# Performance work log

Hardware: AMD Instinct MI355X
Metric: run time of the kernel (lower is better)

## Reference

```python
import jax, jax.numpy as jnp
import numpy as np
import math

B, S, E, R = 128, 16, 512, 500  # batch, seq_len, emb_size, relation_num


def setup_inputs() -> dict:
    key = jax.random.key(0)
    ks = jax.random.split(key, 12)
    s = 1.0 / math.sqrt(E)
    emb = jax.random.normal(ks[0], (R + 1, E), jnp.float32) * s
    emb = emb.at[R].set(0.0)  # padding_idx row is zero in torch
    w_ih = jax.random.normal(ks[1], (4 * E, E), jnp.float32) * s
    w_hh = jax.random.normal(ks[2], (4 * E, E), jnp.float32) * s
    b_ih = jax.random.normal(ks[3], (4 * E,), jnp.float32) * s
    b_hh = jax.random.normal(ks[4], (4 * E,), jnp.float32) * s
    fc_w = jax.random.normal(ks[5], (1, E), jnp.float32) * s
    fc_b = jax.random.normal(ks[6], (1,), jnp.float32) * s
    fcq_w = jax.random.normal(ks[7], (E, E), jnp.float32) * s
    fcq_b = jax.random.normal(ks[8], (E,), jnp.float32) * s
    fck_w = jax.random.normal(ks[9], (E, E), jnp.float32) * s
    fck_b = jax.random.normal(ks[10], (E,), jnp.float32) * s
    tokens = jax.random.randint(ks[11], (B, S), 0, R)  # avoid padding idx R
    return dict(tokens=tokens, emb=emb, w_ih=w_ih, w_hh=w_hh, b_ih=b_ih,
                b_hh=b_hh, fc_w=fc_w, fc_b=fc_b, fcq_w=fcq_w, fcq_b=fcq_b,
                fck_w=fck_w, fck_b=fck_b)


def _lstm_pair(x, w_ih, w_hh, b):
    # x: [..., 2, E]; 2-step LSTM from zero state, return final hidden [..., E]
    def cell(xt, h, c):
        g = xt @ w_ih.T + h @ w_hh.T + b
        i, f, gg, o = jnp.split(g, 4, axis=-1)  # torch gate order i,f,g,o
        c = jax.nn.sigmoid(f) * c + jax.nn.sigmoid(i) * jnp.tanh(gg)
        return jax.nn.sigmoid(o) * jnp.tanh(c), c
    z = jnp.zeros_like(x[..., 0, :])
    h1, c1 = cell(x[..., 0, :], z, z)
    h2, _ = cell(x[..., 1, :], h1, c1)
    return h2


def _attention(x, rel_emb, fcq_w, fcq_b, fck_w, fck_b):
    # x: [B,q,E]; keys = [relation embeddings ; x] -> scores [B,q,R+q]
    b = x.shape[0]
    rel = jnp.broadcast_to(rel_emb[None], (b,) + rel_emb.shape)
    kin = jnp.concatenate([rel, x], axis=1)
    k = kin @ fck_w.T + fck_b
    q = x @ fcq_w.T + fcq_b
    return jnp.einsum('bqe,bke->bqk', q, k) / math.sqrt(E)


def _entropy(scores):
    lp = jax.nn.log_softmax(scores, axis=-1)
    return -jnp.sum(jnp.exp(lp) * lp, axis=-1)


def reference(tokens, emb, w_ih, w_hh, b_ih, b_hh, fc_w, fc_b,
              fcq_w, fcq_b, fck_w, fck_b):
    b_lstm = b_ih + b_hh
    rel_emb = emb[:R]  # relation embeddings used as attention keys/values
    cur = emb[tokens]  # [B,S,E]
    bidx = jnp.arange(B)
    losses = []
    for L in range(S, 1, -1):  # lengths processed: S, S-1, ..., 2
        if L > 2:
            # all adjacent pairs, batched 2-step LSTM: [B, L-1, E]
            pairs = jnp.stack([cur[:, :-1], cur[:, 1:]], axis=2)
            h = _lstm_pair(pairs, w_ih, w_hh, b_lstm)
            sc = jax.nn.sigmoid(h @ fc_w.T + fc_b)[..., 0]  # [B, L-1]
            sel = jnp.argmax(sc, axis=-1)  # [B]
            selected = jnp.take_along_axis(h, sel[:, None, None], axis=1)  # [B,1,E]
            scores = _attention(selected, rel_emb, fcq_w, fcq_b, fck_w, fck_b)
            losses.append(_entropy(scores))  # [B,1]
            # weightedAverage: mask is all-False for seq_len==1, plain softmax
            prob = jax.nn.softmax(scores, axis=-1)  # [B,1,R+1]
            all_emb = jnp.concatenate(
                [jnp.broadcast_to(rel_emb[None], (B, R, E)), selected], axis=1)
            merged = jnp.einsum('bqk,bke->bqe', prob, all_emb)[:, 0]  # [B,E]
            # output = inputs.detach().clone(); write merged at sel; drop row sel+1
            base = jax.lax.stop_gradient(cur)
            base = base.at[bidx, sel].set(merged)
            j = jnp.arange(L - 1)[None, :]
            src = j + (j > sel[:, None]).astype(j.dtype)
            cur = jnp.take_along_axis(base, src[:, :, None], axis=1)  # [B,L-1,E]
        else:  # L == 2: plain LSTM over the two tokens
            h = _lstm_pair(cur, w_ih, w_hh, b_lstm)  # [B,E]
            cur = h[:, None, :]
            losses.append(jnp.zeros((B, 1), cur.dtype))
    scores_f = _attention(cur, rel_emb, fcq_w, fcq_b, fck_w, fck_b)  # [B,1,R+1]
    losses.append(_entropy(scores_f))
    loss_tensor = jnp.concatenate(losses, axis=-1)  # [B,S]
    return scores_f[:, 0], loss_tensor
```

## Files before the change

kernel.cpp:

```cpp
#include <hip/hip_runtime.h>
#include <hip/hip_bf16.h>

#define BB 128
#define SS 16
#define EE 512
#define RR 500
#define G4 2048
#define OUT0 64128
#define NSC 501
#define NPAIR 2047
#define NSU 1012

__device__ __forceinline__ float sigm(float x) { return 1.f / (1.f + expf(-x)); }

__device__ float g_blstm[G4];
__device__ float g_fcw[EE + 4];
__device__ float g_qbias[1024];
__device__ float g_Krel[RR * EE];
__device__ float g_cur[BB * SS * EE];
__device__ float g_G[BB * SS * G4];
__device__ float g_h1[BB * SS * EE];
__device__ float g_c1[BB * SS * EE];
__device__ float g_h2[BB * SS * EE];
__device__ float g_g2[BB * SS * G4];
__device__ float g_sc[BB * SS];
__device__ float g_ent[BB * SS];
__device__ int   g_sel[BB];
__device__ int   g_ord[BB * SS];
__device__ float g_fckwT[EE * EE];
__device__ float g_W2[RR * EE];
__device__ float g_Mx[EE * EE];
__device__ float g_c2[RR + 4];
__device__ float g_v1[EE];
__device__ float g_c0[1];
__device__ float g_su[BB * NSU];

__global__ void k_prep(const float* __restrict__ bih, const float* __restrict__ bhh,
                       const float* __restrict__ fcwv, const float* __restrict__ fcbv,
                       const float* __restrict__ fcqb, const float* __restrict__ fckb) {
    int i = blockIdx.x * blockDim.x + threadIdx.x;
    if (i < G4) g_blstm[i] = bih[i] + bhh[i];
    if (i < EE) {
        g_fcw[i] = fcwv[i];
        g_qbias[i] = fcqb[i];
        g_qbias[EE + i] = fckb[i];
    }
    if (i == 0) g_fcw[EE] = fcbv[0];
    if (i < BB * SS) g_ord[i] = i;
}

__global__ void k_gather(const int* __restrict__ tok, const float* __restrict__ emb) {
    int i = blockIdx.x * blockDim.x + threadIdx.x;
    if (i >= BB * SS * EE) return;
    int e = i & (EE - 1);
    int r = i >> 9;
    int t = tok[r];
    g_cur[i] = emb[(size_t)t * EE + e];
}

__global__ void k_tr(const float* __restrict__ fckw) {
    int i = blockIdx.x * blockDim.x + threadIdx.x;
    if (i >= EE * EE) return;
    int ep = i >> 9;
    int f = i & (EE - 1);
    g_fckwT[(size_t)f * EE + ep] = fckw[(size_t)ep * EE + f];
}

__global__ __launch_bounds__(512) void k_vprep(const float* __restrict__ fcqw, const float* __restrict__ fckw) {
    __shared__ float sh[512];
    int t = threadIdx.x;
    int blk = blockIdx.x;
    if (blk == 0) {
        float acc = 0.f;
        for (int ep = 0; ep < EE; ep++)
            acc += g_qbias[ep] * fckw[(size_t)ep * EE + t] + g_qbias[EE + ep] * fcqw[(size_t)ep * EE + t];
        g_v1[t] = acc;
    } else if (blk == 1) {
        sh[t] = g_qbias[t] * g_qbias[EE + t];
        __syncthreads();
        for (int s = 256; s > 0; s >>= 1) { if (t < s) sh[t] += sh[t + s]; __syncthreads(); }
        if (t == 0) g_c0[0] = sh[0];
    } else {
        int k = blk - 2;
        sh[t] = g_Krel[(size_t)k * EE + t] * g_qbias[t];
        __syncthreads();
        for (int s = 256; s > 0; s >>= 1) { if (t < s) sh[t] += sh[t + s]; __syncthreads(); }
        if (t == 0) g_c2[k] = sh[0];
    }
}

#define TM 32
#define TN 64
#define TK 32
__device__ __forceinline__ void gemm_dev(
    const float* __restrict__ A, int lda,
    const float* __restrict__ W, int ldw, int wtrans,
    const float* __restrict__ bias, const float* __restrict__ Dadd, int ldd,
    float* __restrict__ C, int ldc, int M, int N, int K)
{
    __shared__ __align__(16) float As[TK][TM + 2];
    __shared__ __align__(16) float Ws[TK][TN + 4];
    int tid = threadIdx.x;
    int mt = blockIdx.y * TM;
    int nt = blockIdx.x * TN;
    int tr = tid >> 4;
    int tc = tid & 15;
    float acc[2][4] = {{0.f,0.f,0.f,0.f},{0.f,0.f,0.f,0.f}};

    int ea = tid * 4;
    int ra = ea >> 5;
    int ka = ea & 31;
    int gmA = mt + ra;
    bool rokA = gmA < M;
    int ew = tid * 8;
    int rw = ew >> 5;
    int kw = ew & 31;
    int gnW = nt + rw;
    bool rokW = gnW < N;

    for (int kt = 0; kt < K; kt += TK) {
        #pragma unroll
        for (int i = 0; i < 4; i++) {
            int gk = kt + ka + i;
            float v = 0.f;
            if (rokA && gk < K) v = A[(size_t)gmA * lda + gk];
            As[ka + i][ra] = v;
        }
        #pragma unroll
        for (int i = 0; i < 8; i++) {
            int gk = kt + kw + i;
            float v = 0.f;
            if (rokW && gk < K)
                v = wtrans ? W[(size_t)gk * ldw + gnW] : W[(size_t)gnW * ldw + gk];
            Ws[kw + i][rw] = v;
        }
        __syncthreads();
        #pragma unroll
        for (int kk = 0; kk < TK; kk++) {
            const float2 a = *(const float2*)&As[kk][2 * tr];
            const float4 w = *(const float4*)&Ws[kk][4 * tc];
            acc[0][0] += a.x * w.x; acc[0][1] += a.x * w.y; acc[0][2] += a.x * w.z; acc[0][3] += a.x * w.w;
            acc[1][0] += a.y * w.x; acc[1][1] += a.y * w.y; acc[1][2] += a.y * w.z; acc[1][3] += a.y * w.w;
        }
        __syncthreads();
    }
    #pragma unroll
    for (int i = 0; i < 2; i++) {
        int gm = mt + 2 * tr + i;
        if (gm >= M) continue;
        #pragma unroll
        for (int j = 0; j < 4; j++) {
            int gn = nt + 4 * tc + j;
            if (gn >= N) continue;
            float v = (i == 0) ? ((j == 0) ? acc[0][0] : (j == 1) ? acc[0][1] : (j == 2) ? acc[0][2] : acc[0][3])
                               : ((j == 0) ? acc[1][0] : (j == 1) ? acc[1][1] : (j == 2) ? acc[1][2] : acc[1][3]);
            if (bias) v += bias[gn];
            if (Dadd) v += Dadd[(size_t)gm * ldd + gn];
            C[(size_t)gm * ldc + gn] = v;
        }
    }
}

__global__ __launch_bounds__(256) void kg_Krel(const float* __restrict__ emb, const float* __restrict__ fckw) {
    gemm_dev(emb, EE, fckw, EE, 0, g_qbias + EE, nullptr, 0, g_Krel, EE, RR, EE, EE);
}
__global__ __launch_bounds__(256) void kg_W2(const float* __restrict__ fcqw) {
    gemm_dev(g_Krel, EE, fcqw, EE, 1, nullptr, nullptr, 0, g_W2, EE, RR, EE, EE);
}
__global__ __launch_bounds__(256) void kg_Mx(const float* __restrict__ fcqw) {
    gemm_dev(g_fckwT, EE, fcqw, EE, 1, nullptr, nullptr, 0, g_Mx, EE, EE, EE, EE);
}
__global__ __launch_bounds__(256) void kg_G(const float* __restrict__ wih) {
    gemm_dev(g_cur, EE, wih, EE, 0, g_blstm, nullptr, 0, g_G, G4, BB * SS, G4, EE);
}
__global__ __launch_bounds__(256) void kg_g2(const float* __restrict__ whh) {
    gemm_dev(g_h1, EE, whh, EE, 0, nullptr, g_G + G4, G4, g_g2, G4, NPAIR, G4, EE);
}

__global__ __launch_bounds__(256) void kg_su(int P) {
    __shared__ __align__(16) float As[TK][TM + 2];
    __shared__ __align__(16) float Ws[TK][TN + 4];
    __shared__ int s_phys[TM];
    int tid = threadIdx.x;
    int mt = blockIdx.y * TM;
    int nt = blockIdx.x * TN;
    int tr = tid >> 4;
    int tc = tid & 15;
    float acc[2][4] = {{0.f,0.f,0.f,0.f},{0.f,0.f,0.f,0.f}};

    if (tid < TM) {
        int b = mt + tid;
        float best = -1e30f; int bi = 0;
        for (int p = 0; p < P; p++) {
            float v = g_sc[b * SS + p];
            if (v > best) { best = v; bi = p; }
        }
        s_phys[tid] = g_ord[b * SS + bi];
        if (blockIdx.x == 0) g_sel[b] = bi;
    }
    __syncthreads();

    int ea = tid * 4;
    int ra = ea >> 5;
    int ka = ea & 31;
    int physA = s_phys[ra];
    int ew = tid * 8;
    int rw = ew >> 5;
    int kw = ew & 31;
    int gnW = nt + rw;
    bool rokW = gnW < NSU;
    const float* Wrow = nullptr;
    if (rokW) Wrow = (gnW < RR) ? (g_W2 + (size_t)gnW * EE) : (g_Mx + (size_t)(gnW - RR) * EE);

    for (int kt = 0; kt < EE; kt += TK) {
        #pragma unroll
        for (int i = 0; i < 4; i++)
            As[ka + i][ra] = g_h2[(size_t)physA * EE + kt + ka + i];
        #pragma unroll
        for (int i = 0; i < 8; i++)
            Ws[kw + i][rw] = rokW ? Wrow[kt + kw + i] : 0.f;
        __syncthreads();
        #pragma unroll
        for (int kk = 0; kk < TK; kk++) {
            const float2 a = *(const float2*)&As[kk][2 * tr];
            const float4 w = *(const float4*)&Ws[kk][4 * tc];
            acc[0][0] += a.x * w.x; acc[0][1] += a.x * w.y; acc[0][2] += a.x * w.z; acc[0][3] += a.x * w.w;
            acc[1][0] += a.y * w.x; acc[1][1] += a.y * w.y; acc[1][2] += a.y * w.z; acc[1][3] += a.y * w.w;
        }
        __syncthreads();
    }
    #pragma unroll
    for (int i = 0; i < 2; i++) {
        int gm = mt + 2 * tr + i;
        #pragma unroll
        for (int j = 0; j < 4; j++) {
            int gn = nt + 4 * tc + j;
            if (gn >= NSU) continue;
            float v = (i == 0) ? ((j == 0) ? acc[0][0] : (j == 1) ? acc[0][1] : (j == 2) ? acc[0][2] : acc[0][3])
                               : ((j == 0) ? acc[1][0] : (j == 1) ? acc[1][1] : (j == 2) ? acc[1][2] : acc[1][3]);
            g_su[(size_t)gm * NSU + gn] = v + (gn < RR ? g_c2[gn] : 0.f);
        }
    }
}

__global__ __launch_bounds__(256) void kg_Gi(const float* __restrict__ wih) {
    __shared__ __align__(16) float As[TK][TM + 2];
    __shared__ __align__(16) float Ws[TK][TN + 4];
    __shared__ int s_phys[TM];
    int tid = threadIdx.x;
    int mt = blockIdx.y * TM;
    int nt = blockIdx.x * TN;
    int tr = tid >> 4;
    int tc = tid & 15;
    float acc[2][4] = {{0.f,0.f,0.f,0.f},{0.f,0.f,0.f,0.f}};

    if (tid < TM) {
        int b = mt + tid;
        s_phys[tid] = g_ord[b * SS + g_sel[b]];
    }
    __syncthreads();

    int ea = tid * 4;
    int ra = ea >> 5;
    int ka = ea & 31;
    int physA = s_phys[ra];
    int ew = tid * 8;
    int rw = ew >> 5;
    int kw = ew & 31;
    int gnW = nt + rw;

    for (int kt = 0; kt < EE; kt += TK) {
        #pragma unroll
        for (int i = 0; i < 4; i++)
            As[ka + i][ra] = g_cur[(size_t)physA * EE + kt + ka + i];
        #pragma unroll
        for (int i = 0; i < 8; i++)
            Ws[kw + i][rw] = wih[(size_t)gnW * EE + kt + kw + i];
        __syncthreads();
        #pragma unroll
        for (int kk = 0; kk < TK; kk++) {
            const float2 a = *(const float2*)&As[kk][2 * tr];
            const float4 w = *(const float4*)&Ws[kk][4 * tc];
            acc[0][0] += a.x * w.x; acc[0][1] += a.x * w.y; acc[0][2] += a.x * w.z; acc[0][3] += a.x * w.w;
            acc[1][0] += a.y * w.x; acc[1][1] += a.y * w.y; acc[1][2] += a.y * w.z; acc[1][3] += a.y * w.w;
        }
        __syncthreads();
    }
    #pragma unroll
    for (int i = 0; i < 2; i++) {
        int phys = s_phys[2 * tr + i];
        #pragma unroll
        for (int j = 0; j < 4; j++) {
            int gn = nt + 4 * tc + j;
            float v = (i == 0) ? ((j == 0) ? acc[0][0] : (j == 1) ? acc[0][1] : (j == 2) ? acc[0][2] : acc[0][3])
                               : ((j == 0) ? acc[1][0] : (j == 1) ? acc[1][1] : (j == 2) ? acc[1][2] : acc[1][3]);
            g_G[(size_t)phys * G4 + gn] = v + g_blstm[gn];
        }
    }
}

__global__ void k_h1i() {
    int idx = blockIdx.x * blockDim.x + threadIdx.x;
    if (idx >= BB * EE) return;
    int b = idx >> 9;
    int e = idx & (EE - 1);
    int phys = g_ord[b * SS + g_sel[b]];
    const float* g = g_G + (size_t)phys * G4;
    float c = sigm(g[e]) * tanhf(g[1024 + e]);
    g_c1[(size_t)phys * EE + e] = c;
    g_h1[(size_t)phys * EE + e] = sigm(g[1536 + e]) * tanhf(c);
}

__global__ __launch_bounds__(256) void kg_g2i(const float* __restrict__ whh) {
    __shared__ __align__(16) float As[TK][TM + 2];
    __shared__ __align__(16) float Ws[TK][TN + 4];
    __shared__ int s_physA[TM];
    __shared__ int s_physD[TM];
    int tid = threadIdx.x;
    int mt = blockIdx.y * TM;
    int nt = blockIdx.x * TN;
    int tr = tid >> 4;
    int tc = tid & 15;
    float acc[2][4] = {{0.f,0.f,0.f,0.f},{0.f,0.f,0.f,0.f}};

    if (tid < TM) {
        int gm = mt + tid;
        int b = gm >> 1;
        int p = min(max(g_sel[b] - 1 + (gm & 1), 0), 14);
        s_physA[tid] = g_ord[b * SS + p];
        s_physD[tid] = g_ord[b * SS + p + 1];
    }
    __syncthreads();

    int ea = tid * 4;
    int ra = ea >> 5;
    int ka = ea & 31;
    int physA = s_physA[ra];
    int ew = tid * 8;
    int rw = ew >> 5;
    int kw = ew & 31;
    int gnW = nt + rw;

    for (int kt = 0; kt < EE; kt += TK) {
        #pragma unroll
        for (int i = 0; i < 4; i++)
            As[ka + i][ra] = g_h1[(size_t)physA * EE + kt + ka + i];
        #pragma unroll
        for (int i = 0; i < 8; i++)
            Ws[kw + i][rw] = whh[(size_t)gnW * EE + kt + kw + i];
        __syncthreads();
        #pragma unroll
        for (int kk = 0; kk < TK; kk++) {
            const float2 a = *(const float2*)&As[kk][2 * tr];
            const float4 w = *(const float4*)&Ws[kk][4 * tc];
            acc[0][0] += a.x * w.x; acc[0][1] += a.x * w.y; acc[0][2] += a.x * w.z; acc[0][3] += a.x * w.w;
            acc[1][0] += a.y * w.x; acc[1][1] += a.y * w.y; acc[1][2] += a.y * w.z; acc[1][3] += a.y * w.w;
        }
        __syncthreads();
    }
    #pragma unroll
    for (int i = 0; i < 2; i++) {
        int gm = mt + 2 * tr + i;
        size_t drow = (size_t)s_physD[2 * tr + i] * G4;
        #pragma unroll
        for (int j = 0; j < 4; j++) {
            int gn = nt + 4 * tc + j;
            float v = (i == 0) ? ((j == 0) ? acc[0][0] : (j == 1) ? acc[0][1] : (j == 2) ? acc[0][2] : acc[0][3])
                               : ((j == 0) ? acc[1][0] : (j == 1) ? acc[1][1] : (j == 2) ? acc[1][2] : acc[1][3]);
            g_g2[(size_t)gm * G4 + gn] = v + g_G[drow + gn];
        }
    }
}

__global__ void k_h1() {
    int idx = blockIdx.x * blockDim.x + threadIdx.x;
    if (idx >= BB * SS * EE) return;
    int m = idx >> 9;
    int e = idx & (EE - 1);
    const float* g = g_G + (size_t)m * G4;
    float c = sigm(g[e]) * tanhf(g[1024 + e]);
    g_c1[idx] = c;
    g_h1[idx] = sigm(g[1536 + e]) * tanhf(c);
}

__global__ __launch_bounds__(256) void k_h2() {
    int m = blockIdx.x;
    const float* g = g_g2 + (size_t)m * G4;
    __shared__ float red[256];
    float part = 0.f;
    for (int e = threadIdx.x; e < EE; e += 256) {
        float c = sigm(g[512 + e]) * g_c1[(size_t)m * EE + e] + sigm(g[e]) * tanhf(g[1024 + e]);
        float h = sigm(g[1536 + e]) * tanhf(c);
        g_h2[(size_t)m * EE + e] = h;
        part += h * g_fcw[e];
    }
    red[threadIdx.x] = part;
    __syncthreads();
    for (int s = 128; s > 0; s >>= 1) {
        if (threadIdx.x < s) red[threadIdx.x] += red[threadIdx.x + s];
        __syncthreads();
    }
    if (threadIdx.x == 0) g_sc[m] = sigm(red[0] + g_fcw[EE]);
}

__global__ __launch_bounds__(256) void k_h2i(int L) {
    int m = blockIdx.x;
    int b = m >> 1;
    int t = m & 1;
    int s = g_sel[b];
    int p = s - 1 + t;
    bool valid = t == 0 ? (s >= 1) : (s <= L - 3);
    if (!valid) return;
    int physL = g_ord[b * SS + p];
    const float* g = g_g2 + (size_t)m * G4;
    __shared__ float red[256];
    float part = 0.f;
    for (int e = threadIdx.x; e < EE; e += 256) {
        float c = sigm(g[512 + e]) * g_c1[(size_t)physL * EE + e] + sigm(g[e]) * tanhf(g[1024 + e]);
        float h = sigm(g[1536 + e]) * tanhf(c);
        g_h2[(size_t)physL * EE + e] = h;
        part += h * g_fcw[e];
    }
    red[threadIdx.x] = part;
    __syncthreads();
    for (int ss = 128; ss > 0; ss >>= 1) {
        if (threadIdx.x < ss) red[threadIdx.x] += red[threadIdx.x + ss];
        __syncthreads();
    }
    if (threadIdx.x == 0) g_sc[b * SS + p] = sigm(red[0] + g_fcw[EE]);
}

__global__ __launch_bounds__(512) void k_smu(int col, int finalFlag, int L,
                                             const float* __restrict__ emb, float* __restrict__ out) {
    int b = blockIdx.x;
    int t = threadIdx.x;
    __shared__ float sh[512];
    __shared__ float srow[NSC];
    __shared__ float s_p500;
    const float* su = g_su + (size_t)b * NSU;
    int s = g_sel[b];
    int phys = g_ord[b * SS + s];
    const float* h2row = g_h2 + (size_t)phys * EE;
    const float isq = 0.044194173824159216f;

    float hv = h2row[t];
    sh[t] = hv * (su[RR + t] + g_v1[t]);
    __syncthreads();
    for (int ss = 256; ss > 0; ss >>= 1) { if (t < ss) sh[t] += sh[t + ss]; __syncthreads(); }
    if (t == 0) srow[RR] = (sh[0] + g_c0[0]) * isq;
    __syncthreads();
    if (t < RR) srow[t] = su[t] * isq;
    __syncthreads();
    float mx = (t < NSC) ? srow[t] : -1e30f;
    sh[t] = mx; __syncthreads();
    for (int ss = 256; ss > 0; ss >>= 1) { if (t < ss) sh[t] = fmaxf(sh[t], sh[t + ss]); __syncthreads(); }
    mx = sh[0]; __syncthreads();
    float zp = (t < NSC) ? expf(srow[t] - mx) : 0.f;
    sh[t] = zp; __syncthreads();
    for (int ss = 256; ss > 0; ss >>= 1) { if (t < ss) sh[t] += sh[t + ss]; __syncthreads(); }
    float lse = mx + logf(sh[0]);
    __syncthreads();
    float p = (t < NSC) ? expf(srow[t] - lse) : 0.f;
    float ep = (t < NSC) ? p * (lse - srow[t]) : 0.f;
    if (finalFlag && t < NSC) out[(size_t)b * NSC + t] = srow[t];
    sh[t] = ep; __syncthreads();
    for (int ss = 256; ss > 0; ss >>= 1) { if (t < ss) sh[t] += sh[t + ss]; __syncthreads(); }
    if (finalFlag) {
        if (t < 16) {
            float v = (t == 15) ? sh[0] : ((t == 14) ? 0.f : g_ent[b * SS + t]);
            out[OUT0 + b * 16 + t] = v;
        }
        return;
    }
    if (t == 0) g_ent[b * SS + col] = sh[0];

    __syncthreads();
    if (t < NSC) srow[t] = p;
    if (t == RR) s_p500 = p;
    __syncthreads();
    float macc = 0.f;
    #pragma unroll 4
    for (int k = 0; k < RR; k++) macc += srow[k] * emb[(size_t)k * EE + t];
    g_cur[(size_t)phys * EE + t] = macc + s_p500 * hv;
    if (t == 0) {
        for (int j = s + 1; j <= L - 2; j++) g_ord[b * SS + j] = g_ord[b * SS + j + 1];
        for (int pp = s + 1; pp <= L - 3; pp++) g_sc[b * SS + pp] = g_sc[b * SS + pp + 1];
    }
}

extern "C" void kernel_launch(void* const* d_in, const int* in_sizes, int n_in,
                              void* d_out, int out_size, void* d_ws, size_t ws_size,
                              hipStream_t stream) {
    const int*   tokens = (const int*)d_in[0];
    const float* emb    = (const float*)d_in[1];
    const float* wih    = (const float*)d_in[2];
    const float* whh    = (const float*)d_in[3];
    const float* bih    = (const float*)d_in[4];
    const float* bhh    = (const float*)d_in[5];
    const float* fcwv   = (const float*)d_in[6];
    const float* fcbv   = (const float*)d_in[7];
    const float* fcqw   = (const float*)d_in[8];
    const float* fcqb   = (const float*)d_in[9];
    const float* fckw   = (const float*)d_in[10];
    const float* fckb   = (const float*)d_in[11];
    float* out = (float*)d_out;

    auto grid32 = [](int M, int N) { return dim3((unsigned)((N + TN - 1) / TN), (unsigned)((M + TM - 1) / TM)); };

    k_prep<<<dim3(8), dim3(256), 0, stream>>>(bih, bhh, fcwv, fcbv, fcqb, fckb);
    kg_Krel<<<grid32(RR, EE), dim3(256), 0, stream>>>(emb, fckw);
    k_tr<<<dim3((EE * EE + 255) / 256), dim3(256), 0, stream>>>(fckw);
    kg_W2<<<grid32(RR, EE), dim3(256), 0, stream>>>(fcqw);
    kg_Mx<<<grid32(EE, EE), dim3(256), 0, stream>>>(fcqw);
    k_vprep<<<dim3(502), dim3(512), 0, stream>>>(fcqw, fckw);
    k_gather<<<dim3((BB * SS * EE + 255) / 256), dim3(256), 0, stream>>>(tokens, emb);

    kg_G<<<grid32(BB * SS, G4), dim3(256), 0, stream>>>(wih);
    k_h1<<<dim3((BB * SS * EE + 255) / 256), dim3(256), 0, stream>>>();
    kg_g2<<<grid32(NPAIR, G4), dim3(256), 0, stream>>>(whh);
    k_h2<<<dim3(NPAIR), dim3(256), 0, stream>>>();

    for (int L = SS; L >= 3; L--) {
        kg_su<<<grid32(BB, NSU), dim3(256), 0, stream>>>(L - 1);
        k_smu<<<dim3(BB), dim3(512), 0, stream>>>(SS - L, 0, L, emb, out);
        kg_Gi<<<grid32(BB, G4), dim3(256), 0, stream>>>(wih);
        k_h1i<<<dim3((BB * EE + 255) / 256), dim3(256), 0, stream>>>();
        kg_g2i<<<grid32(2 * BB, G4), dim3(256), 0, stream>>>(whh);
        k_h2i<<<dim3(2 * BB), dim3(256), 0, stream>>>(L);
    }

    kg_su<<<grid32(BB, NSU), dim3(256), 0, stream>>>(1);
    k_smu<<<dim3(BB), dim3(512), 0, stream>>>(15, 1, 2, emb, out);

    (void)in_sizes; (void)n_in; (void)out_size; (void)d_ws; (void)ws_size;
}
```

Before: 2.051 ms.

## Use 128x128 register-blocked GEMM tiles for the large LSTM gate GEMMs

```diff
diff --git a/kernel.cpp b/kernel.cpp
--- a/kernel.cpp
+++ b/kernel.cpp
@@ -161,6 +161,102 @@
     }
 }
 
+#define UM 128
+#define UN 128
+#define UK 32
+__device__ __forceinline__ void gemm_dev128(
+    const float* __restrict__ A, int lda,
+    const float* __restrict__ W, int ldw,
+    const float* __restrict__ bias, const float* __restrict__ Dadd, int ldd,
+    float* __restrict__ C, int ldc, int M, int N, int K)
+{
+    __shared__ __align__(16) float As[UK][UM + 4];
+    __shared__ __align__(16) float Ws[UK][UN + 4];
+    int tid = threadIdx.x;
+    int mt = blockIdx.y * UM;
+    int nt = blockIdx.x * UN;
+    int tr = tid >> 4;
+    int tc = tid & 15;
+    float acc[8][8] = {};
+
+    int ra = tid & 127;
+    int ka = (tid >> 7) << 4;
+    int gmA = mt + ra;
+    bool rokA = gmA < M;
+    int gnW = nt + ra;
+    bool rokW = gnW < N;
+    const float* Arow = A + (size_t)(rokA ? gmA : 0) * lda;
+    const float* Wrow = W + (size_t)(rokW ? gnW : 0) * ldw;
+
+    for (int kt = 0; kt < K; kt += UK) {
+        if (rokA) {
+            const float4 a0 = *(const float4*)&Arow[kt + ka];
+            const float4 a1 = *(const float4*)&Arow[kt + ka + 4];
+            const float4 a2 = *(const float4*)&Arow[kt + ka + 8];
+            const float4 a3 = *(const float4*)&Arow[kt + ka + 12];
+            As[ka +  0][ra] = a0.x; As[ka +  1][ra] = a0.y; As[ka +  2][ra] = a0.z; As[ka +  3][ra] = a0.w;
+            As[ka +  4][ra] = a1.x; As[ka +  5][ra] = a1.y; As[ka +  6][ra] = a1.z; As[ka +  7][ra] = a1.w;
+            As[ka +  8][ra] = a2.x; As[ka +  9][ra] = a2.y; As[ka + 10][ra] = a2.z; As[ka + 11][ra] = a2.w;
+            As[ka + 12][ra] = a3.x; As[ka + 13][ra] = a3.y; As[ka + 14][ra] = a3.z; As[ka + 15][ra] = a3.w;
+        } else {
+            #pragma unroll
+            for (int i = 0; i < 16; i++) As[ka + i][ra] = 0.f;
+        }
+        if (rokW) {
+            const float4 w0 = *(const float4*)&Wrow[kt + ka];
+            const float4 w1 = *(const float4*)&Wrow[kt + ka + 4];
+            const float4 w2 = *(const float4*)&Wrow[kt + ka + 8];
+            const float4 w3 = *(const float4*)&Wrow[kt + ka + 12];
+            Ws[ka +  0][ra] = w0.x; Ws[ka +  1][ra] = w0.y; Ws[ka +  2][ra] = w0.z; Ws[ka +  3][ra] = w0.w;
+            Ws[ka +  4][ra] = w1.x; Ws[ka +  5][ra] = w1.y; Ws[ka +  6][ra] = w1.z; Ws[ka +  7][ra] = w1.w;
+            Ws[ka +  8][ra] = w2.x; Ws[ka +  9][ra] = w2.y; Ws[ka + 10][ra] = w2.z; Ws[ka + 11][ra] = w2.w;
+            Ws[ka + 12][ra] = w3.x; Ws[ka + 13][ra] = w3.y; Ws[ka + 14][ra] = w3.z; Ws[ka + 15][ra] = w3.w;
+        } else {
+            #pragma unroll
+            for (int i = 0; i < 16; i++) Ws[ka + i][ra] = 0.f;
+        }
+        __syncthreads();
+        #pragma unroll
+        for (int kk = 0; kk < UK; kk++) {
+            const float4 aA = *(const float4*)&As[kk][8 * tr];
+            const float4 aB = *(const float4*)&As[kk][8 * tr + 4];
+            const float4 wA = *(const float4*)&Ws[kk][8 * tc];
+            const float4 wB = *(const float4*)&Ws[kk][8 * tc + 4];
+            const float am[8] = {aA.x, aA.y, aA.z, aA.w, aB.x, aB.y, aB.z, aB.w};
+            const float wn[8] = {wA.x, wA.y, wA.z, wA.w, wB.x, wB.y, wB.z, wB.w};
+            #pragma unroll
+            for (int i = 0; i < 8; i++)
+                #pragma unroll
+                for (int j = 0; j < 8; j++)
+                    acc[i][j] += am[i] * wn[j];
+        }
+        __syncthreads();
+    }
+
+    float4 b0 = {0.f, 0.f, 0.f, 0.f}, b1 = {0.f, 0.f, 0.f, 0.f};
+    int gn0 = nt + 8 * tc;
+    if (bias) {
+        b0 = *(const float4*)&bias[gn0];
+        b1 = *(const float4*)&bias[gn0 + 4];
+    }
+    #pragma unroll
+    for (int i = 0; i < 8; i++) {
+        int gm = mt + 8 * tr + i;
+        if (gm >= M) continue;
+        float4 v0, v1;
+        v0.x = acc[i][0] + b0.x; v0.y = acc[i][1] + b0.y; v0.z = acc[i][2] + b0.z; v0.w = acc[i][3] + b0.w;
+        v1.x = acc[i][4] + b1.x; v1.y = acc[i][5] + b1.y; v1.z = acc[i][6] + b1.z; v1.w = acc[i][7] + b1.w;
+        if (Dadd) {
+            const float4 d0 = *(const float4*)&Dadd[(size_t)gm * ldd + gn0];
+            const float4 d1 = *(const float4*)&Dadd[(size_t)gm * ldd + gn0 + 4];
+            v0.x += d0.x; v0.y += d0.y; v0.z += d0.z; v0.w += d0.w;
+            v1.x += d1.x; v1.y += d1.y; v1.z += d1.z; v1.w += d1.w;
+        }
+        *(float4*)&C[(size_t)gm * ldc + gn0] = v0;
+        *(float4*)&C[(size_t)gm * ldc + gn0 + 4] = v1;
+    }
+}
+
 __global__ __launch_bounds__(256) void kg_Krel(const float* __restrict__ emb, const float* __restrict__ fckw) {
     gemm_dev(emb, EE, fckw, EE, 0, g_qbias + EE, nullptr, 0, g_Krel, EE, RR, EE, EE);
 }
@@ -171,10 +267,10 @@
     gemm_dev(g_fckwT, EE, fcqw, EE, 1, nullptr, nullptr, 0, g_Mx, EE, EE, EE, EE);
 }
 __global__ __launch_bounds__(256) void kg_G(const float* __restrict__ wih) {
-    gemm_dev(g_cur, EE, wih, EE, 0, g_blstm, nullptr, 0, g_G, G4, BB * SS, G4, EE);
+    gemm_dev128(g_cur, EE, wih, EE, g_blstm, nullptr, 0, g_G, G4, BB * SS, G4, EE);
 }
 __global__ __launch_bounds__(256) void kg_g2(const float* __restrict__ whh) {
-    gemm_dev(g_h1, EE, whh, EE, 0, nullptr, g_G + G4, G4, g_g2, G4, NPAIR, G4, EE);
+    gemm_dev128(g_h1, EE, whh, EE, nullptr, g_G + G4, G4, g_g2, G4, NPAIR, G4, EE);
 }
 
 __global__ __launch_bounds__(256) void kg_su(int P) {
@@ -506,6 +602,7 @@
     float* out = (float*)d_out;
 
     auto grid32 = [](int M, int N) { return dim3((unsigned)((N + TN - 1) / TN), (unsigned)((M + TM - 1) / TM)); };
+    auto grid128 = [](int M, int N) { return dim3((unsigned)((N + UN - 1) / UN), (unsigned)((M + UM - 1) / UM)); };
 
     k_prep<<<dim3(8), dim3(256), 0, stream>>>(bih, bhh, fcwv, fcbv, fcqb, fckb);
     kg_Krel<<<grid32(RR, EE), dim3(256), 0, stream>>>(emb, fckw);
@@ -515,9 +612,9 @@
     k_vprep<<<dim3(502), dim3(512), 0, stream>>>(fcqw, fckw);
     k_gather<<<dim3((BB * SS * EE + 255) / 256), dim3(256), 0, stream>>>(tokens, emb);
 
-    kg_G<<<grid32(BB * SS, G4), dim3(256), 0, stream>>>(wih);
+    kg_G<<<grid128(BB * SS, G4), dim3(256), 0, stream>>>(wih);
     k_h1<<<dim3((BB * SS * EE + 255) / 256), dim3(256), 0, stream>>>();
-    kg_g2<<<grid32(NPAIR, G4), dim3(256), 0, stream>>>(whh);
+    kg_g2<<<grid128(NPAIR, G4), dim3(256), 0, stream>>>(whh);
     k_h2<<<dim3(NPAIR), dim3(256), 0, stream>>>();
 
     for (int L = SS; L >= 3; L--) {
```

Result: no change. 2.050 ms (-0.0%).

## Interleave LSTM gate weights to fuse cell updates into GEMM epilogues

Applied to the files above, without the earlier changes.

```diff
diff --git a/kernel.cpp b/kernel.cpp
--- a/kernel.cpp
+++ b/kernel.cpp
@@ -14,6 +14,9 @@
 __device__ __forceinline__ float sigm(float x) { return 1.f / (1.f + expf(-x)); }
 
 __device__ float g_blstm[G4];
+__device__ float g_blstmr[G4];
+__device__ float g_wihr[G4 * EE];
+__device__ float g_whhr[G4 * EE];
 __device__ float g_fcw[EE + 4];
 __device__ float g_qbias[1024];
 __device__ float g_Krel[RR * EE];
@@ -22,7 +25,6 @@
 __device__ float g_h1[BB * SS * EE];
 __device__ float g_c1[BB * SS * EE];
 __device__ float g_h2[BB * SS * EE];
-__device__ float g_g2[BB * SS * G4];
 __device__ float g_sc[BB * SS];
 __device__ float g_ent[BB * SS];
 __device__ int   g_sel[BB];
@@ -47,6 +49,19 @@
     }
     if (i == 0) g_fcw[EE] = fcbv[0];
     if (i < BB * SS) g_ord[i] = i;
+}
+
+__global__ void k_reord(const float* __restrict__ wih, const float* __restrict__ whh) {
+    int i = blockIdx.x * blockDim.x + threadIdx.x;
+    if (i >= G4 * EE) return;
+    int n = i >> 9;
+    int k = i & (EE - 1);
+    int e = n & (EE - 1);
+    int gate = n >> 9;
+    int np = 4 * e + gate;
+    g_wihr[(size_t)np * EE + k] = wih[i];
+    g_whhr[(size_t)np * EE + k] = whh[i];
+    if (k == 0) g_blstmr[np] = g_blstm[n];
 }
 
 __global__ void k_gather(const int* __restrict__ tok, const float* __restrict__ emb) {
@@ -161,6 +176,116 @@
     }
 }
 
+#define UM 128
+#define UN 128
+#define UK 32
+template<int MODE>
+__global__ __launch_bounds__(256) void kg_bigF() {
+    __shared__ __align__(16) float As[UK][UM + 4];
+    __shared__ __align__(16) float Ws[UK][UN + 4];
+    const float* __restrict__ A = (MODE == 0) ? g_cur : g_h1;
+    const float* __restrict__ W = (MODE == 0) ? g_wihr : g_whhr;
+    const int M = (MODE == 0) ? (BB * SS) : NPAIR;
+    int tid = threadIdx.x;
+    int mt = blockIdx.y * UM;
+    int nt = blockIdx.x * UN;
+    int tr = tid >> 4;
+    int tc = tid & 15;
+    float acc[8][8] = {};
+
+    int ra = tid & 127;
+    int ka = (tid >> 7) << 4;
+    int gmA = mt + ra;
+    bool rokA = gmA < M;
+    const float* Arow = A + (size_t)(rokA ? gmA : 0) * EE;
+    const float* Wrow = W + (size_t)(nt + ra) * EE;
+
+    float4 pa[4] = {{0,0,0,0},{0,0,0,0},{0,0,0,0},{0,0,0,0}};
+    float4 pw[4];
+    #pragma unroll
+    for (int j = 0; j < 4; j++) {
+        if (rokA) pa[j] = *(const float4*)&Arow[ka + 4 * j];
+        pw[j] = *(const float4*)&Wrow[ka + 4 * j];
+    }
+
+    for (int kt = 0; kt < EE; kt += UK) {
+        __syncthreads();
+        #pragma unroll
+        for (int j = 0; j < 4; j++) {
+            As[ka + 4 * j + 0][ra] = pa[j].x;
+            As[ka + 4 * j + 1][ra] = pa[j].y;
+            As[ka + 4 * j + 2][ra] = pa[j].z;
+            As[ka + 4 * j + 3][ra] = pa[j].w;
+            Ws[ka + 4 * j + 0][ra] = pw[j].x;
+            Ws[ka + 4 * j + 1][ra] = pw[j].y;
+            Ws[ka + 4 * j + 2][ra] = pw[j].z;
+            Ws[ka + 4 * j + 3][ra] = pw[j].w;
+        }
+        __syncthreads();
+        if (kt + UK < EE) {
+            int k2 = kt + UK + ka;
+            #pragma unroll
+            for (int j = 0; j < 4; j++) {
+                if (rokA) pa[j] = *(const float4*)&Arow[k2 + 4 * j];
+                pw[j] = *(const float4*)&Wrow[k2 + 4 * j];
+            }
+        }
+        #pragma unroll
+        for (int kk = 0; kk < UK; kk++) {
+            const float4 aA = *(const float4*)&As[kk][4 * tr];
+            const float4 aB = *(const float4*)&As[kk][64 + 4 * tr];
+            const float4 wA = *(const float4*)&Ws[kk][4 * tc];
+            const float4 wB = *(const float4*)&Ws[kk][64 + 4 * tc];
+            const float am[8] = {aA.x, aA.y, aA.z, aA.w, aB.x, aB.y, aB.z, aB.w};
+            const float wn[8] = {wA.x, wA.y, wA.z, wA.w, wB.x, wB.y, wB.z, wB.w};
+            #pragma unroll
+            for (int i = 0; i < 8; i++)
+                #pragma unroll
+                for (int j = 0; j < 8; j++)
+                    acc[i][j] += am[i] * wn[j];
+        }
+    }
+
+    int c0 = nt + 4 * tc;
+    int c1c = c0 + 64;
+    int e0 = (nt >> 2) + tc;
+    #pragma unroll
+    for (int ri = 0; ri < 8; ri++) {
+        int row = (ri < 4) ? (4 * tr + ri) : (60 + 4 * tr + ri);
+        int gm = mt + row;
+        if (gm >= M) continue;
+        float q0x = acc[ri][0], q0y = acc[ri][1], q0z = acc[ri][2], q0w = acc[ri][3];
+        float q1x = acc[ri][4], q1y = acc[ri][5], q1z = acc[ri][6], q1w = acc[ri][7];
+        if (MODE == 0) {
+            const float4 b0 = *(const float4*)&g_blstmr[c0];
+            const float4 b1 = *(const float4*)&g_blstmr[c1c];
+            q0x += b0.x; q0y += b0.y; q0z += b0.z; q0w += b0.w;
+            q1x += b1.x; q1y += b1.y; q1z += b1.z; q1w += b1.w;
+            float4 o0 = {q0x, q0y, q0z, q0w};
+            float4 o1 = {q1x, q1y, q1z, q1w};
+            *(float4*)&g_G[(size_t)gm * G4 + c0]  = o0;
+            *(float4*)&g_G[(size_t)gm * G4 + c1c] = o1;
+            float cA = sigm(q0x) * tanhf(q0z);
+            g_c1[(size_t)gm * EE + e0] = cA;
+            g_h1[(size_t)gm * EE + e0] = sigm(q0w) * tanhf(cA);
+            float cB = sigm(q1x) * tanhf(q1z);
+            g_c1[(size_t)gm * EE + e0 + 16] = cB;
+            g_h1[(size_t)gm * EE + e0 + 16] = sigm(q1w) * tanhf(cB);
+        } else {
+            const float4 d0 = *(const float4*)&g_G[(size_t)(gm + 1) * G4 + c0];
+            const float4 d1 = *(const float4*)&g_G[(size_t)(gm + 1) * G4 + c1c];
+            q0x += d0.x; q0y += d0.y; q0z += d0.z; q0w += d0.w;
+            q1x += d1.x; q1y += d1.y; q1z += d1.z; q1w += d1.w;
+            float c1a = g_c1[(size_t)gm * EE + e0];
+            float c1b = g_c1[(size_t)gm * EE + e0 + 16];
+            float cA = sigm(q0y) * c1a + sigm(q0x) * tanhf(q0z);
+            g_h2[(size_t)gm * EE + e0] = sigm(q0w) * tanhf(cA);
+            float cB = sigm(q1y) * c1b + sigm(q1x) * tanhf(q1z);
+            g_h2[(size_t)gm * EE + e0 + 16] = sigm(q1w) * tanhf(cB);
+        }
+    }
+}
+
 __global__ __launch_bounds__(256) void kg_Krel(const float* __restrict__ emb, const float* __restrict__ fckw) {
     gemm_dev(emb, EE, fckw, EE, 0, g_qbias + EE, nullptr, 0, g_Krel, EE, RR, EE, EE);
 }
@@ -170,11 +295,36 @@
 __global__ __launch_bounds__(256) void kg_Mx(const float* __restrict__ fcqw) {
     gemm_dev(g_fckwT, EE, fcqw, EE, 1, nullptr, nullptr, 0, g_Mx, EE, EE, EE, EE);
 }
-__global__ __launch_bounds__(256) void kg_G(const float* __restrict__ wih) {
-    gemm_dev(g_cur, EE, wih, EE, 0, g_blstm, nullptr, 0, g_G, G4, BB * SS, G4, EE);
-}
-__global__ __launch_bounds__(256) void kg_g2(const float* __restrict__ whh) {
-    gemm_dev(g_h1, EE, whh, EE, 0, nullptr, g_G + G4, G4, g_g2, G4, NPAIR, G4, EE);
+
+__global__ __launch_bounds__(256) void k_scI() {
+    int m = blockIdx.x;
+    int t = threadIdx.x;
+    __shared__ float red[256];
+    const float* h = g_h2 + (size_t)m * EE;
+    float part = h[t] * g_fcw[t] + h[t + 256] * g_fcw[t + 256];
+    red[t] = part;
+    __syncthreads();
+    for (int s = 128; s > 0; s >>= 1) { if (t < s) red[t] += red[t + s]; __syncthreads(); }
+    if (t == 0) g_sc[m] = red[0];
+}
+
+__global__ __launch_bounds__(256) void k_scP(int L) {
+    int m = blockIdx.x;
+    int b = m >> 1;
+    int tcand = m & 1;
+    int s = g_sel[b];
+    int p = s - 1 + tcand;
+    bool valid = tcand == 0 ? (s >= 1) : (s <= L - 3);
+    if (!valid) return;
+    int physL = g_ord[b * SS + p];
+    int t = threadIdx.x;
+    __shared__ float red[256];
+    const float* h = g_h2 + (size_t)physL * EE;
+    float part = h[t] * g_fcw[t] + h[t + 256] * g_fcw[t + 256];
+    red[t] = part;
+    __syncthreads();
+    for (int s2 = 128; s2 > 0; s2 >>= 1) { if (t < s2) red[t] += red[t + s2]; __syncthreads(); }
+    if (t == 0) g_sc[b * SS + p] = red[0];
 }
 
 __global__ __launch_bounds__(256) void kg_su(int P) {
@@ -243,7 +393,7 @@
     }
 }
 
-__global__ __launch_bounds__(256) void kg_Gi(const float* __restrict__ wih) {
+__global__ __launch_bounds__(256) void kg_GiF() {
     __shared__ __align__(16) float As[TK][TM + 2];
     __shared__ __align__(16) float Ws[TK][TN + 4];
     __shared__ int s_phys[TM];
@@ -275,7 +425,7 @@
             As[ka + i][ra] = g_cur[(size_t)physA * EE + kt + ka + i];
         #pragma unroll
         for (int i = 0; i < 8; i++)
-            Ws[kw + i][rw] = wih[(size_t)gnW * EE + kt + kw + i];
+            Ws[kw + i][rw] = g_wihr[(size_t)gnW * EE + kt + kw + i];
         __syncthreads();
         #pragma unroll
         for (int kk = 0; kk < TK; kk++) {
@@ -286,36 +436,30 @@
         }
         __syncthreads();
     }
+    int c0 = nt + 4 * tc;
+    int e0 = (nt >> 2) + tc;
+    const float4 b4 = *(const float4*)&g_blstmr[c0];
     #pragma unroll
     for (int i = 0; i < 2; i++) {
         int phys = s_phys[2 * tr + i];
-        #pragma unroll
-        for (int j = 0; j < 4; j++) {
-            int gn = nt + 4 * tc + j;
-            float v = (i == 0) ? ((j == 0) ? acc[0][0] : (j == 1) ? acc[0][1] : (j == 2) ? acc[0][2] : acc[0][3])
-                               : ((j == 0) ? acc[1][0] : (j == 1) ? acc[1][1] : (j == 2) ? acc[1][2] : acc[1][3]);
-            g_G[(size_t)phys * G4 + gn] = v + g_blstm[gn];
-        }
-    }
-}
-
-__global__ void k_h1i() {
-    int idx = blockIdx.x * blockDim.x + threadIdx.x;
-    if (idx >= BB * EE) return;
-    int b = idx >> 9;
-    int e = idx & (EE - 1);
-    int phys = g_ord[b * SS + g_sel[b]];
-    const float* g = g_G + (size_t)phys * G4;
-    float c = sigm(g[e]) * tanhf(g[1024 + e]);
-    g_c1[(size_t)phys * EE + e] = c;
-    g_h1[(size_t)phys * EE + e] = sigm(g[1536 + e]) * tanhf(c);
-}
-
-__global__ __launch_bounds__(256) void kg_g2i(const float* __restrict__ whh) {
+        float qx = acc[i][0] + b4.x;
+        float qy = acc[i][1] + b4.y;
+        float qz = acc[i][2] + b4.z;
+        float qw = acc[i][3] + b4.w;
+        float4 o = {qx, qy, qz, qw};
+        *(float4*)&g_G[(size_t)phys * G4 + c0] = o;
+        float cA = sigm(qx) * tanhf(qz);
+        g_c1[(size_t)phys * EE + e0] = cA;
+        g_h1[(size_t)phys * EE + e0] = sigm(qw) * tanhf(cA);
+    }
+}
+
+__global__ __launch_bounds__(256) void kg_g2iF(int L) {
     __shared__ __align__(16) float As[TK][TM + 2];
     __shared__ __align__(16) float Ws[TK][TN + 4];
     __shared__ int s_physA[TM];
     __shared__ int s_physD[TM];
+    __shared__ int s_val[TM];
     int tid = threadIdx.x;
     int mt = blockIdx.y * TM;
     int nt = blockIdx.x * TN;
@@ -326,9 +470,12 @@
     if (tid < TM) {
         int gm = mt + tid;
         int b = gm >> 1;
-        int p = min(max(g_sel[b] - 1 + (gm & 1), 0), 14);
+        int tcand = gm & 1;
+        int s = g_sel[b];
+        int p = min(max(s - 1 + tcand, 0), 14);
         s_physA[tid] = g_ord[b * SS + p];
         s_physD[tid] = g_ord[b * SS + p + 1];
+        s_val[tid] = tcand == 0 ? (s >= 1) : (s <= L - 3);
     }
     __syncthreads();
 
@@ -347,7 +494,7 @@
             As[ka + i][ra] = g_h1[(size_t)physA * EE + kt + ka + i];
         #pragma unroll
         for (int i = 0; i < 8; i++)
-            Ws[kw + i][rw] = whh[(size_t)gnW * EE + kt + kw + i];
+            Ws[kw + i][rw] = g_whhr[(size_t)gnW * EE + kt + kw + i];
         __syncthreads();
         #pragma unroll
         for (int kk = 0; kk < TK; kk++) {
@@ -358,76 +505,23 @@
         }
         __syncthreads();
     }
+    int c0 = nt + 4 * tc;
+    int e0 = (nt >> 2) + tc;
     #pragma unroll
     for (int i = 0; i < 2; i++) {
-        int gm = mt + 2 * tr + i;
-        size_t drow = (size_t)s_physD[2 * tr + i] * G4;
-        #pragma unroll
-        for (int j = 0; j < 4; j++) {
-            int gn = nt + 4 * tc + j;
-            float v = (i == 0) ? ((j == 0) ? acc[0][0] : (j == 1) ? acc[0][1] : (j == 2) ? acc[0][2] : acc[0][3])
-                               : ((j == 0) ? acc[1][0] : (j == 1) ? acc[1][1] : (j == 2) ? acc[1][2] : acc[1][3]);
-            g_g2[(size_t)gm * G4 + gn] = v + g_G[drow + gn];
-        }
-    }
-}
-
-__global__ void k_h1() {
-    int idx = blockIdx.x * blockDim.x + threadIdx.x;
-    if (idx >= BB * SS * EE) return;
-    int m = idx >> 9;
-    int e = idx & (EE - 1);
-    const float* g = g_G + (size_t)m * G4;
-    float c = sigm(g[e]) * tanhf(g[1024 + e]);
-    g_c1[idx] = c;
-    g_h1[idx] = sigm(g[1536 + e]) * tanhf(c);
-}
-
-__global__ __launch_bounds__(256) void k_h2() {
-    int m = blockIdx.x;
-    const float* g = g_g2 + (size_t)m * G4;
-    __shared__ float red[256];
-    float part = 0.f;
-    for (int e = threadIdx.x; e < EE; e += 256) {
-        float c = sigm(g[512 + e]) * g_c1[(size_t)m * EE + e] + sigm(g[e]) * tanhf(g[1024 + e]);
-        float h = sigm(g[1536 + e]) * tanhf(c);
-        g_h2[(size_t)m * EE + e] = h;
-        part += h * g_fcw[e];
-    }
-    red[threadIdx.x] = part;
-    __syncthreads();
-    for (int s = 128; s > 0; s >>= 1) {
-        if (threadIdx.x < s) red[threadIdx.x] += red[threadIdx.x + s];
-        __syncthreads();
-    }
-    if (threadIdx.x == 0) g_sc[m] = sigm(red[0] + g_fcw[EE]);
-}
-
-__global__ __launch_bounds__(256) void k_h2i(int L) {
-    int m = blockIdx.x;
-    int b = m >> 1;
-    int t = m & 1;
-    int s = g_sel[b];
-    int p = s - 1 + t;
-    bool valid = t == 0 ? (s >= 1) : (s <= L - 3);
-    if (!valid) return;
-    int physL = g_ord[b * SS + p];
-    const float* g = g_g2 + (size_t)m * G4;
-    __shared__ float red[256];
-    float part = 0.f;
-    for (int e = threadIdx.x; e < EE; e += 256) {
-        float c = sigm(g[512 + e]) * g_c1[(size_t)physL * EE + e] + sigm(g[e]) * tanhf(g[1024 + e]);
-        float h = sigm(g[1536 + e]) * tanhf(c);
-        g_h2[(size_t)physL * EE + e] = h;
-        part += h * g_fcw[e];
-    }
-    red[threadIdx.x] = part;
-    __syncthreads();
-    for (int ss = 128; ss > 0; ss >>= 1) {
-        if (threadIdx.x < ss) red[threadIdx.x] += red[threadIdx.x + ss];
-        __syncthreads();
-    }
-    if (threadIdx.x == 0) g_sc[b * SS + p] = sigm(red[0] + g_fcw[EE]);
+        int r = 2 * tr + i;
+        if (!s_val[r]) continue;
+        int pA = s_physA[r];
+        int pD = s_physD[r];
+        const float4 d4 = *(const float4*)&g_G[(size_t)pD * G4 + c0];
+        float qx = acc[i][0] + d4.x;
+        float qy = acc[i][1] + d4.y;
+        float qz = acc[i][2] + d4.z;
+        float qw = acc[i][3] + d4.w;
+        float c1v = g_c1[(size_t)pA * EE + e0];
+        float cA = sigm(qy) * c1v + sigm(qx) * tanhf(qz);
+        g_h2[(size_t)pA * EE + e0] = sigm(qw) * tanhf(cA);
+    }
 }
 
 __global__ __launch_bounds__(512) void k_smu(int col, int finalFlag, int L,
@@ -508,6 +602,7 @@
     auto grid32 = [](int M, int N) { return dim3((unsigned)((N + TN - 1) / TN), (unsigned)((M + TM - 1) / TM)); };
 
     k_prep<<<dim3(8), dim3(256), 0, stream>>>(bih, bhh, fcwv, fcbv, fcqb, fckb);
+    k_reord<<<dim3((G4 * EE) / 256), dim3(256), 0, stream>>>(wih, whh);
     kg_Krel<<<grid32(RR, EE), dim3(256), 0, stream>>>(emb, fckw);
     k_tr<<<dim3((EE * EE + 255) / 256), dim3(256), 0, stream>>>(fckw);
     kg_W2<<<grid32(RR, EE), dim3(256), 0, stream>>>(fcqw);
@@ -515,18 +610,16 @@
     k_vprep<<<dim3(502), dim3(512), 0, stream>>>(fcqw, fckw);
     k_gather<<<dim3((BB * SS * EE + 255) / 256), dim3(256), 0, stream>>>(tokens, emb);
 
-    kg_G<<<grid32(BB * SS, G4), dim3(256), 0, stream>>>(wih);
-    k_h1<<<dim3((BB * SS * EE + 255) / 256), dim3(256), 0, stream>>>();
-    kg_g2<<<grid32(NPAIR, G4), dim3(256), 0, stream>>>(whh);
-    k_h2<<<dim3(NPAIR), dim3(256), 0, stream>>>();
+    kg_bigF<0><<<dim3(16, 16), dim3(256), 0, stream>>>();
+    kg_bigF<1><<<dim3(16, 16), dim3(256), 0, stream>>>();
+    k_scI<<<dim3(NPAIR), dim3(256), 0, stream>>>();
 
     for (int L = SS; L >= 3; L--) {
         kg_su<<<grid32(BB, NSU), dim3(256), 0, stream>>>(L - 1);
         k_smu<<<dim3(BB), dim3(512), 0, stream>>>(SS - L, 0, L, emb, out);
-        kg_Gi<<<grid32(BB, G4), dim3(256), 0, stream>>>(wih);
-        k_h1i<<<dim3((BB * EE + 255) / 256), dim3(256), 0, stream>>>();
-        kg_g2i<<<grid32(2 * BB, G4), dim3(256), 0, stream>>>(whh);
-        k_h2i<<<dim3(2 * BB), dim3(256), 0, stream>>>(L);
+        kg_GiF<<<grid32(BB, G4), dim3(256), 0, stream>>>();
+        kg_g2iF<<<grid32(2 * BB, G4), dim3(256), 0, stream>>>(L);
+        k_scP<<<dim3(2 * BB), dim3(256), 0, stream>>>(L);
     }
 
     kg_su<<<grid32(BB, NSU), dim3(256), 0, stream>>>(1);
```

New measurement: 1.953 ms. 1.05x faster.
